# Kernel tuning notes

Hardware: AMD Instinct MI355X
Metric: run time of the kernel (lower is better)

Reference implementation:

```python
import jax, jax.numpy as jnp
import numpy as np

T, H, E, I = 2048, 2048, 8, 1408

def setup_inputs() -> dict:
    key = jax.random.key(0)
    k1, k2, k3, k4 = jax.random.split(key, 4)
    x = jax.random.normal(k1, (T, H), dtype=jnp.float32)
    gate_w = jax.random.normal(k2, (H, E), dtype=jnp.float32) * (1.0 / np.sqrt(H))
    w1 = jax.random.normal(k3, (E, H, I), dtype=jnp.float32) * (1.0 / np.sqrt(H))
    w2 = jax.random.normal(k4, (E, I, H), dtype=jnp.float32) * (1.0 / np.sqrt(I))
    return {"x": x, "gate_w": gate_w, "w1": w1, "w2": w2, "topk": 2}


def reference(x, gate_w, w1, w2, topk):
    # Router: logits -> softmax (fp32) -> top-k -> renormalize (fused_moe default)
    logits = x @ gate_w                                   # [T, E]
    probs = jax.nn.softmax(logits.astype(jnp.float32), axis=-1)
    tk_w, tk_i = jax.lax.top_k(probs, topk)               # [T, k]
    tk_w = tk_w / jnp.sum(tk_w, axis=-1, keepdims=True)
    # Scatter top-k weights into dense [T, E] combine matrix (zeros elsewhere)
    t_idx = jnp.arange(x.shape[0])[:, None]
    w_full = jnp.zeros(probs.shape, probs.dtype).at[t_idx, tk_i].set(tk_w)
    # Expert MLP: silu(x @ w1[e]) @ w2[e], combined with routing weights
    mid = jnp.einsum('th,ehi->tei', x, w1)                # [T, E, I]
    y = jnp.einsum('tei,eih->teh', jax.nn.silu(mid), w2)  # [T, E, H]
    out = jnp.einsum('te,teh->th', w_full.astype(x.dtype), y)
    return out
```

## Files before the change

### kernel.cpp

```cpp
#include <hip/hip_runtime.h>
#include <hip/hip_bf16.h>
#include <math.h>

#define TT 2048
#define HH 2048
#define EE 8
#define II 1408
#define PMAX 4608
#define MAXTILES 48

typedef short bf16x8 __attribute__((ext_vector_type(8)));
typedef float f32x4 __attribute__((ext_vector_type(4)));
typedef unsigned int u32;
typedef unsigned short u16;

__device__ __forceinline__ u16 f2bf(float f) {
  union { float f; u32 u; } v; v.f = f;
  u32 r = v.u + 0x7fffu + ((v.u >> 16) & 1u);
  return (u16)(r >> 16);
}

__device__ __forceinline__ float bf2f(u16 b) {
  union { u32 u; float f; } v; v.u = ((u32)b) << 16; return v.f;
}

__device__ __forceinline__ void gload16(const void* g, void* l) {
  __builtin_amdgcn_global_load_lds((const __attribute__((address_space(1))) u32*)g,
                                   (__attribute__((address_space(3))) u32*)l, 16, 0, 0);
}

__global__ void router_kernel(const float* __restrict__ x, const float* __restrict__ gw,
                              int* __restrict__ tk_id, float* __restrict__ tk_w) {
  int t = blockIdx.x;
  int lane = threadIdx.x;
  float acc[EE];
#pragma unroll
  for (int e = 0; e < EE; ++e) acc[e] = 0.f;
  const float* xr = x + (size_t)t * HH;
  for (int h = lane; h < HH; h += 64) {
    float xv = xr[h];
    const float* g = gw + (size_t)h * EE;
#pragma unroll
    for (int e = 0; e < EE; ++e) acc[e] += xv * g[e];
  }
#pragma unroll
  for (int off = 32; off > 0; off >>= 1) {
#pragma unroll
    for (int e = 0; e < EE; ++e) acc[e] += __shfl_down(acc[e], off, 64);
  }
  if (lane == 0) {
    int i0 = 0;
#pragma unroll
    for (int e = 1; e < EE; ++e) if (acc[e] > acc[i0]) i0 = e;
    int i1 = (i0 == 0) ? 1 : 0;
#pragma unroll
    for (int e = 0; e < EE; ++e) { if (e == i0) continue; if (acc[e] > acc[i1]) i1 = e; }
    float d = acc[i1] - acc[i0];
    float p1 = expf(d);
    float w0 = 1.f / (1.f + p1);
    float w1v = p1 * w0;
    tk_id[2 * t] = i0; tk_id[2 * t + 1] = i1;
    tk_w[2 * t] = w0;  tk_w[2 * t + 1] = w1v;
  }
}

__global__ void scanassign_kernel(const int* __restrict__ tk_id, const float* __restrict__ tk_w,
                                  int* __restrict__ offsets, int* __restrict__ poff,
                                  int* __restrict__ tok_list, float* __restrict__ wt_list,
                                  int* __restrict__ islot,
                                  int* __restrict__ t_row0, int* __restrict__ t_e,
                                  int* __restrict__ t_rlim) {
  __shared__ int s_cnt[EE];
  __shared__ int s_off[EE + 1];
  __shared__ int s_poff[EE + 1];
  __shared__ int s_cur[EE];
  int tid = threadIdx.x;
  if (tid < EE) { s_cnt[tid] = 0; s_cur[tid] = 0; }
  __syncthreads();
  for (int i = tid; i < 2 * TT; i += 256) atomicAdd(&s_cnt[tk_id[i]], 1);
  __syncthreads();
  if (tid == 0) {
    int s = 0, ps = 0;
    for (int e = 0; e < EE; ++e) {
      s_off[e] = s; s_poff[e] = ps;
      s += s_cnt[e];
      ps += ((s_cnt[e] + 63) >> 6) << 6;
    }
    s_off[EE] = s; s_poff[EE] = ps;
    for (int e = 0; e <= EE; ++e) { offsets[e] = s_off[e]; poff[e] = s_poff[e]; }
    int nt = 0;
    for (int e = 0; e < EE; ++e) {
      for (int r0 = s_poff[e]; r0 < s_poff[e + 1]; r0 += 128) {
        t_row0[nt] = r0; t_e[nt] = e; t_rlim[nt] = s_poff[e + 1]; ++nt;
      }
    }
    for (int i = nt; i < MAXTILES; ++i) t_row0[i] = -1;
  }
  __syncthreads();
  for (int t = tid; t < TT; t += 256) {
#pragma unroll
    for (int k = 0; k < 2; ++k) {
      int e = tk_id[2 * t + k];
      int p = atomicAdd(&s_cur[e], 1);
      tok_list[s_off[e] + p] = t;
      wt_list[s_off[e] + p] = tk_w[2 * t + k];
      islot[2 * t + k] = s_poff[e] + p;
    }
  }
}

__global__ void gather_x_kernel(const float* __restrict__ x, const int* __restrict__ tok_list,
                                const int* __restrict__ offsets, const int* __restrict__ poff,
                                u16* __restrict__ xg) {
  int p = blockIdx.x;
  if (p >= poff[EE]) return;
  int e = 0;
#pragma unroll
  for (int q = 1; q < EE; ++q) if (p >= poff[q]) e = q;
  int cnt = offsets[e + 1] - offsets[e];
  int r = p - poff[e]; if (r >= cnt) r = cnt - 1;
  int tok = tok_list[offsets[e] + r];
  int c = threadIdx.x * 8;
  float4 v0 = *(const float4*)(x + (size_t)tok * HH + c);
  float4 v1 = *(const float4*)(x + (size_t)tok * HH + c + 4);
  u16 o[8] = { f2bf(v0.x), f2bf(v0.y), f2bf(v0.z), f2bf(v0.w),
               f2bf(v1.x), f2bf(v1.y), f2bf(v1.z), f2bf(v1.w) };
  *(uint4*)(xg + (size_t)p * HH + c) = *(uint4*)o;
}

__global__ void convtrans_kernel(const float* __restrict__ w, u16* __restrict__ wb,
                                 int K, int N) {
  int e = blockIdx.z;
  int n0 = blockIdx.x * 64, k0 = blockIdx.y * 64;
  __shared__ u16 sT[64][72];
  const float* we = w + (size_t)e * K * N;
  u16* wbe = wb + (size_t)e * K * N;
  int tid = threadIdx.x;
  int kl = tid >> 4, n4 = tid & 15;
#pragma unroll
  for (int j = 0; j < 4; ++j) {
    int k = kl + j * 16;
    float4 v = *(const float4*)(we + (size_t)(k0 + k) * N + n0 + n4 * 4);
    sT[n4 * 4 + 0][k] = f2bf(v.x);
    sT[n4 * 4 + 1][k] = f2bf(v.y);
    sT[n4 * 4 + 2][k] = f2bf(v.z);
    sT[n4 * 4 + 3][k] = f2bf(v.w);
  }
  __syncthreads();
  int nl = tid >> 3, kc = tid & 7;
#pragma unroll
  for (int j = 0; j < 2; ++j) {
    int n = nl + j * 32;
    uint4 v = *(const uint4*)(&sT[n][kc * 8]);
    *(uint4*)(wbe + (size_t)(n0 + n) * K + k0 + kc * 8) = v;
  }
}

__global__ void combine_kernel(const u16* __restrict__ y, const int* __restrict__ islot,
                               const float* __restrict__ tk_w, float* __restrict__ out) {
  int t = blockIdx.x;
  int h = threadIdx.x * 8;
  int s0 = islot[2 * t], s1 = islot[2 * t + 1];
  float w0 = tk_w[2 * t], w1 = tk_w[2 * t + 1];
  uint4 a = *(const uint4*)(y + (size_t)s0 * HH + h);
  uint4 b = *(const uint4*)(y + (size_t)s1 * HH + h);
  const u16* ap = (const u16*)&a;
  const u16* bp = (const u16*)&b;
  float* op = out + (size_t)t * HH + h;
  float4 r0, r1;
  r0.x = w0 * bf2f(ap[0]) + w1 * bf2f(bp[0]);
  r0.y = w0 * bf2f(ap[1]) + w1 * bf2f(bp[1]);
  r0.z = w0 * bf2f(ap[2]) + w1 * bf2f(bp[2]);
  r0.w = w0 * bf2f(ap[3]) + w1 * bf2f(bp[3]);
  r1.x = w0 * bf2f(ap[4]) + w1 * bf2f(bp[4]);
  r1.y = w0 * bf2f(ap[5]) + w1 * bf2f(bp[5]);
  r1.z = w0 * bf2f(ap[6]) + w1 * bf2f(bp[6]);
  r1.w = w0 * bf2f(ap[7]) + w1 * bf2f(bp[7]);
  *(float4*)(op) = r0;
  *(float4*)(op + 4) = r1;
}

template <int KDIM, int MODE>
__launch_bounds__(256)
__global__ void moe_gemm128(const u16* __restrict__ A, const u16* __restrict__ B,
                            const int* __restrict__ t_row0, const int* __restrict__ t_e,
                            const int* __restrict__ t_rlim,
                            u16* __restrict__ midB, u16* __restrict__ y) {
  constexpr int Ndim = (MODE == 2) ? HH : II;
  constexpr int NCB = Ndim / 64;
  constexpr int NT = KDIM / 64;

  int L = blockIdx.x;
  int xcd = L & 7;
  int q = L >> 3;
  int g = q / NCB;
  int n0b = q - g * NCB;
  int ti = g * 8 + xcd;
  int row0 = t_row0[ti];
  if (row0 < 0) return;
  int e = t_e[ti];
  int rlim = t_rlim[ti];
  int n0 = n0b * 64;

  __shared__ u16 sA[128][64];
  __shared__ u16 sB[64][64];

  int tid = threadIdx.x;
  int lane = tid & 63, wv = tid >> 6;
  int wm = wv >> 1, wn = wv & 1;
  int fr = lane & 15, kg = lane >> 4;

  int rA = lane >> 3;
  int colsw = ((lane & 7) ^ rA) * 8;
  const u16* Abase = A + (size_t)(row0 + rA) * KDIM + colsw;
  const u16* Bbase = B + (size_t)e * (size_t)Ndim * KDIM + (size_t)(n0 + rA) * KDIM + colsw;

  f32x4 acc[4][2];
#pragma unroll
  for (int m = 0; m < 4; ++m)
#pragma unroll
    for (int n = 0; n < 2; ++n)
      acc[m][n] = (f32x4){0.f, 0.f, 0.f, 0.f};

  for (int t = 0; t < NT; ++t) {
    int kof = t * 64;
#pragma unroll
    for (int j = 0; j < 4; ++j) {
      int c = wv * 4 + j;
      gload16(Abase + (size_t)c * 8 * KDIM + kof, &sA[c * 8][0]);
    }
#pragma unroll
    for (int j = 0; j < 2; ++j) {
      int c = wv * 2 + j;
      gload16(Bbase + (size_t)c * 8 * KDIM + kof, &sB[c * 8][0]);
    }
    __syncthreads();
#pragma unroll
    for (int kh = 0; kh < 2; ++kh) {
      bf16x8 af[4], bg[2];
      int cbyte = (kh * 64 + kg * 16) ^ ((fr & 7) << 4);
#pragma unroll
      for (int m = 0; m < 4; ++m)
        af[m] = *(const bf16x8*)((const char*)&sA[0][0] + (wm * 64 + m * 16 + fr) * 128 + cbyte);
#pragma unroll
      for (int n = 0; n < 2; ++n)
        bg[n] = *(const bf16x8*)((const char*)&sB[0][0] + (wn * 32 + n * 16 + fr) * 128 + cbyte);
#pragma unroll
      for (int m = 0; m < 4; ++m)
#pragma unroll
        for (int n = 0; n < 2; ++n)
          acc[m][n] = __builtin_amdgcn_mfma_f32_16x16x32_bf16(af[m], bg[n], acc[m][n], 0, 0, 0);
    }
    __syncthreads();
  }

#pragma unroll
  for (int m = 0; m < 4; ++m) {
    int lr = wm * 64 + m * 16 + kg * 4;
#pragma unroll
    for (int n = 0; n < 2; ++n) {
      int lc = wn * 32 + n * 16 + fr;
#pragma unroll
      for (int r = 0; r < 4; ++r) {
        int rr = row0 + lr + r;
        if (rr < rlim) {
          if constexpr (MODE == 0) {
            float v = acc[m][n][r];
            float s = v / (1.f + expf(-v));
            midB[(size_t)rr * II + n0 + lc] = f2bf(s);
          } else {
            y[(size_t)rr * HH + n0 + lc] = f2bf(acc[m][n][r]);
          }
        }
      }
    }
  }
}

__global__ void zero_kernel(float4* __restrict__ out4, int n4) {
  int i = blockIdx.x * blockDim.x + threadIdx.x;
  int stride = gridDim.x * blockDim.x;
  float4 z; z.x = 0.f; z.y = 0.f; z.z = 0.f; z.w = 0.f;
  for (int j = i; j < n4; j += stride) out4[j] = z;
}

__launch_bounds__(256, 2)
__global__ void gemm1_small(const float* __restrict__ x, const float* __restrict__ w1,
                            const int* __restrict__ tok_list, const int* __restrict__ offsets,
                            u16* __restrict__ mid) {
  int e = blockIdx.z;
  int g_off = offsets[e];
  int n_e = offsets[e + 1] - g_off;
  int row0 = blockIdx.y * 64;
  if (row0 >= n_e) return;
  int n0 = blockIdx.x * 64;
  __shared__ u16 sA[64][72];
  __shared__ u16 sB[64][72];
  __shared__ int s_tok[64];
  int tid = threadIdx.x;
  if (tid < 64) {
    int r = row0 + tid;
    s_tok[tid] = tok_list[g_off + ((r < n_e) ? r : (n_e - 1))];
  }
  __syncthreads();
  int lane = tid & 63;
  int wv = tid >> 6;
  int wm = wv >> 1, wn = wv & 1;
  int fr = lane & 15, kg = lane >> 4;
  f32x4 acc[2][2];
#pragma unroll
  for (int i = 0; i < 2; ++i)
#pragma unroll
    for (int j = 0; j < 2; ++j) acc[i][j] = (f32x4){0.f, 0.f, 0.f, 0.f};
  const float* w1e = w1 + (size_t)e * HH * II;
  for (int k0 = 0; k0 < HH; k0 += 64) {
#pragma unroll
    for (int i = 0; i < 4; ++i) {
      int idx = tid + i * 256;
      int r = idx >> 4, c4 = idx & 15;
      float4 v = *(const float4*)(x + (size_t)s_tok[r] * HH + k0 + c4 * 4);
      unsigned long long pk = (unsigned long long)f2bf(v.x)
                            | ((unsigned long long)f2bf(v.y) << 16)
                            | ((unsigned long long)f2bf(v.z) << 32)
                            | ((unsigned long long)f2bf(v.w) << 48);
      *(unsigned long long*)(&sA[r][c4 * 4]) = pk;
    }
#pragma unroll
    for (int i = 0; i < 4; ++i) {
      int idx = tid + i * 256;
      int kk = idx >> 4, c4 = idx & 15;
      float4 v = *(const float4*)(w1e + (size_t)(k0 + kk) * II + n0 + c4 * 4);
      sB[c4 * 4 + 0][kk] = f2bf(v.x);
      sB[c4 * 4 + 1][kk] = f2bf(v.y);
      sB[c4 * 4 + 2][kk] = f2bf(v.z);
      sB[c4 * 4 + 3][kk] = f2bf(v.w);
    }
    __syncthreads();
#pragma unroll
    for (int kk = 0; kk < 64; kk += 32) {
      bf16x8 af[2], bg[2];
#pragma unroll
      for (int m = 0; m < 2; ++m) af[m] = *(const bf16x8*)(&sA[wm * 32 + m * 16 + fr][kk + kg * 8]);
#pragma unroll
      for (int n = 0; n < 2; ++n) bg[n] = *(const bf16x8*)(&sB[wn * 32 + n * 16 + fr][kk + kg * 8]);
#pragma unroll
      for (int m = 0; m < 2; ++m)
#pragma unroll
        for (int n = 0; n < 2; ++n)
          acc[m][n] = __builtin_amdgcn_mfma_f32_16x16x32_bf16(af[m], bg[n], acc[m][n], 0, 0, 0);
    }
    __syncthreads();
  }
#pragma unroll
  for (int m = 0; m < 2; ++m)
#pragma unroll
    for (int n = 0; n < 2; ++n)
#pragma unroll
      for (int r = 0; r < 4; ++r) {
        int lr = wm * 32 + m * 16 + kg * 4 + r;
        int lc = wn * 32 + n * 16 + fr;
        if (row0 + lr < n_e) {
          float v = acc[m][n][r];
          float s = v / (1.f + expf(-v));
          mid[(size_t)(g_off + row0 + lr) * II + n0 + lc] = f2bf(s);
        }
      }
}

__launch_bounds__(256, 2)
__global__ void gemm2_small(const u16* __restrict__ mid, const float* __restrict__ w2,
                            const int* __restrict__ tok_list, const float* __restrict__ wt_list,
                            const int* __restrict__ offsets, float* __restrict__ out) {
  int e = blockIdx.z;
  int g_off = offsets[e];
  int n_e = offsets[e + 1] - g_off;
  int row0 = blockIdx.y * 64;
  if (row0 >= n_e) return;
  int n0 = blockIdx.x * 64;
  __shared__ u16 sA[64][72];
  __shared__ u16 sB[64][72];
  __shared__ int s_tok[64];
  __shared__ float s_wt[64];
  int tid = threadIdx.x;
  if (tid < 64) {
    int r = row0 + tid;
    int cr = (r < n_e) ? r : (n_e - 1);
    s_tok[tid] = tok_list[g_off + cr];
    s_wt[tid] = wt_list[g_off + cr];
  }
  __syncthreads();
  int lane = tid & 63;
  int wv = tid >> 6;
  int wm = wv >> 1, wn = wv & 1;
  int fr = lane & 15, kg = lane >> 4;
  f32x4 acc[2][2];
#pragma unroll
  for (int i = 0; i < 2; ++i)
#pragma unroll
    for (int j = 0; j < 2; ++j) acc[i][j] = (f32x4){0.f, 0.f, 0.f, 0.f};
  const float* w2e = w2 + (size_t)e * II * HH;
  for (int k0 = 0; k0 < II; k0 += 64) {
#pragma unroll
    for (int i = 0; i < 2; ++i) {
      int idx = tid + i * 256;
      int r = idx >> 3, c8 = idx & 7;
      int gr = row0 + r; if (gr >= n_e) gr = n_e - 1;
      uint4 v = *(const uint4*)(mid + (size_t)(g_off + gr) * II + k0 + c8 * 8);
      *(uint4*)(&sA[r][c8 * 8]) = v;
    }
#pragma unroll
    for (int i = 0; i < 4; ++i) {
      int idx = tid + i * 256;
      int kk = idx >> 4, c4 = idx & 15;
      float4 v = *(const float4*)(w2e + (size_t)(k0 + kk) * HH + n0 + c4 * 4);
      sB[c4 * 4 + 0][kk] = f2bf(v.x);
      sB[c4 * 4 + 1][kk] = f2bf(v.y);
      sB[c4 * 4 + 2][kk] = f2bf(v.z);
      sB[c4 * 4 + 3][kk] = f2bf(v.w);
    }
    __syncthreads();
#pragma unroll
    for (int kk = 0; kk < 64; kk += 32) {
      bf16x8 af[2], bg[2];
#pragma unroll
      for (int m = 0; m < 2; ++m) af[m] = *(const bf16x8*)(&sA[wm * 32 + m * 16 + fr][kk + kg * 8]);
#pragma unroll
      for (int n = 0; n < 2; ++n) bg[n] = *(const bf16x8*)(&sB[wn * 32 + n * 16 + fr][kk + kg * 8]);
#pragma unroll
      for (int m = 0; m < 2; ++m)
#pragma unroll
        for (int n = 0; n < 2; ++n)
          acc[m][n] = __builtin_amdgcn_mfma_f32_16x16x32_bf16(af[m], bg[n], acc[m][n], 0, 0, 0);
    }
    __syncthreads();
  }
#pragma unroll
  for (int m = 0; m < 2; ++m)
#pragma unroll
    for (int n = 0; n < 2; ++n)
#pragma unroll
      for (int r = 0; r < 4; ++r) {
        int lr = wm * 32 + m * 16 + kg * 4 + r;
        int lc = wn * 32 + n * 16 + fr;
        if (row0 + lr < n_e) {
          float v = acc[m][n][r] * s_wt[lr];
          atomicAdd(out + (size_t)s_tok[lr] * HH + n0 + lc, v);
        }
      }
}

extern "C" void kernel_launch(void* const* d_in, const int* in_sizes, int n_in,
                              void* d_out, int out_size, void* d_ws, size_t ws_size,
                              hipStream_t stream) {
  const float* x  = (const float*)d_in[0];
  const float* gw = (const float*)d_in[1];
  const float* w1 = (const float*)d_in[2];
  const float* w2 = (const float*)d_in[3];
  float* out = (float*)d_out;

  char* ws = (char*)d_ws;
  int*   tk_id    = (int*)(ws);
  float* tk_w     = (float*)(ws + 16384);
  int*   offsets  = (int*)(ws + 32832);
  int*   poff     = (int*)(ws + 32896);
  int*   tok_list = (int*)(ws + 33024);
  float* wt_list  = (float*)(ws + 49408);
  int*   islot    = (int*)(ws + 65792);
  int*   t_row0   = (int*)(ws + 98304);
  int*   t_e      = (int*)(ws + 98560);
  int*   t_rlim   = (int*)(ws + 98816);

  u16* xg    = (u16*)(ws + (1u << 20));
  u16* midBp = (u16*)(ws + (20u << 20));
  u16* w1b   = (u16*)(ws + (33u << 20));
  u16* w2b   = (u16*)(ws + 80740352u);
  u16* y     = (u16*)(ws + (33u << 20));
  const size_t NEED = 126877696u;

  router_kernel<<<TT, 64, 0, stream>>>(x, gw, tk_id, tk_w);
  scanassign_kernel<<<1, 256, 0, stream>>>(tk_id, tk_w, offsets, poff, tok_list, wt_list,
                                           islot, t_row0, t_e, t_rlim);

  if (ws_size >= NEED) {
    gather_x_kernel<<<PMAX, 256, 0, stream>>>(x, tok_list, offsets, poff, xg);
    convtrans_kernel<<<dim3(II / 64, HH / 64, EE), 256, 0, stream>>>(w1, w1b, HH, II);
    convtrans_kernel<<<dim3(HH / 64, II / 64, EE), 256, 0, stream>>>(w2, w2b, II, HH);
    moe_gemm128<HH, 0><<<MAXTILES * (II / 64), 256, 0, stream>>>(
        xg, w1b, t_row0, t_e, t_rlim, midBp, y);
    moe_gemm128<II, 2><<<MAXTILES * (HH / 64), 256, 0, stream>>>(
        midBp, w2b, t_row0, t_e, t_rlim, midBp, y);
    combine_kernel<<<TT, 256, 0, stream>>>(y, islot, tk_w, out);
  } else {
    u16* mid0 = (u16*)(ws + 131072);
    zero_kernel<<<1024, 256, 0, stream>>>((float4*)out, TT * HH / 4);
    gemm1_small<<<dim3(II / 64, TT / 64, EE), 256, 0, stream>>>(x, w1, tok_list, offsets, mid0);
    gemm2_small<<<dim3(HH / 64, TT / 64, EE), 256, 0, stream>>>(mid0, w2, tok_list, wt_list, offsets, out);
  }
}
```

Baseline: 192.4 us.

## Co-schedule weight conversion with router and first GEMM in shared launches

The w1 fp32-to-bf16 transpose is merged into the router launch, and the w2 conversion is merged into the first expert GEMM launch as extra blocks. Independent work now runs concurrently and the number of kernel launches drops. The router also moves from one wave per block to four tokens per 256-thread block. The trade-off is that the GEMM1 blocks now share a launch with memory-bound conversion blocks, which can affect scheduling and occupancy.

Result: faster. 176.2 us (-8.4%).

```diff
diff --git a/kernel.cpp b/kernel.cpp
--- a/kernel.cpp
+++ b/kernel.cpp
@@ -8,6 +8,8 @@
 #define II 1408
 #define PMAX 4608
 #define MAXTILES 48
+#define G1TILES (MAXTILES * (II / 64))
+#define NCONV 5632
 
 typedef short bf16x8 __attribute__((ext_vector_type(8)));
 typedef float f32x4 __attribute__((ext_vector_type(4)));
@@ -29,38 +31,74 @@
                                    (__attribute__((address_space(3))) u32*)l, 16, 0, 0);
 }
 
-__global__ void router_kernel(const float* __restrict__ x, const float* __restrict__ gw,
-                              int* __restrict__ tk_id, float* __restrict__ tk_w) {
-  int t = blockIdx.x;
-  int lane = threadIdx.x;
-  float acc[EE];
-#pragma unroll
-  for (int e = 0; e < EE; ++e) acc[e] = 0.f;
-  const float* xr = x + (size_t)t * HH;
-  for (int h = lane; h < HH; h += 64) {
-    float xv = xr[h];
-    const float* g = gw + (size_t)h * EE;
-#pragma unroll
-    for (int e = 0; e < EE; ++e) acc[e] += xv * g[e];
-  }
-#pragma unroll
-  for (int off = 32; off > 0; off >>= 1) {
-#pragma unroll
-    for (int e = 0; e < EE; ++e) acc[e] += __shfl_down(acc[e], off, 64);
-  }
-  if (lane == 0) {
-    int i0 = 0;
-#pragma unroll
-    for (int e = 1; e < EE; ++e) if (acc[e] > acc[i0]) i0 = e;
-    int i1 = (i0 == 0) ? 1 : 0;
-#pragma unroll
-    for (int e = 0; e < EE; ++e) { if (e == i0) continue; if (acc[e] > acc[i1]) i1 = e; }
-    float d = acc[i1] - acc[i0];
-    float p1 = expf(d);
-    float w0 = 1.f / (1.f + p1);
-    float w1v = p1 * w0;
-    tk_id[2 * t] = i0; tk_id[2 * t + 1] = i1;
-    tk_w[2 * t] = w0;  tk_w[2 * t + 1] = w1v;
+__device__ __forceinline__ void conv_block(const float* __restrict__ w, u16* __restrict__ wb,
+                                           int K, int N, int b, u16* smem) {
+  int nx = N / 64, ky = K / 64;
+  int n0 = (b % nx) * 64;
+  int k0 = ((b / nx) % ky) * 64;
+  int e  = b / (nx * ky);
+  u16 (*sT)[72] = (u16(*)[72])smem;
+  const float* we = w + (size_t)e * K * N;
+  u16* wbe = wb + (size_t)e * K * N;
+  int tid = threadIdx.x;
+  int kl = tid >> 4, n4 = tid & 15;
+#pragma unroll
+  for (int j = 0; j < 4; ++j) {
+    int k = kl + j * 16;
+    float4 v = *(const float4*)(we + (size_t)(k0 + k) * N + n0 + n4 * 4);
+    sT[n4 * 4 + 0][k] = f2bf(v.x);
+    sT[n4 * 4 + 1][k] = f2bf(v.y);
+    sT[n4 * 4 + 2][k] = f2bf(v.z);
+    sT[n4 * 4 + 3][k] = f2bf(v.w);
+  }
+  __syncthreads();
+  int nl = tid >> 3, kc = tid & 7;
+#pragma unroll
+  for (int j = 0; j < 2; ++j) {
+    int n = nl + j * 32;
+    uint4 v = *(const uint4*)(&sT[n][kc * 8]);
+    *(uint4*)(wbe + (size_t)(n0 + n) * K + k0 + kc * 8) = v;
+  }
+}
+
+__global__ void router_conv_kernel(const float* __restrict__ x, const float* __restrict__ gw,
+                                   int* __restrict__ tk_id, float* __restrict__ tk_w,
+                                   const float* __restrict__ w1, u16* __restrict__ w1b) {
+  __shared__ u16 smem[64 * 72];
+  if (blockIdx.x < TT / 4) {
+    int wv = threadIdx.x >> 6, lane = threadIdx.x & 63;
+    int t = blockIdx.x * 4 + wv;
+    float acc[EE];
+#pragma unroll
+    for (int e = 0; e < EE; ++e) acc[e] = 0.f;
+    const float* xr = x + (size_t)t * HH;
+    for (int h = lane; h < HH; h += 64) {
+      float xv = xr[h];
+      const float* g = gw + (size_t)h * EE;
+#pragma unroll
+      for (int e = 0; e < EE; ++e) acc[e] += xv * g[e];
+    }
+#pragma unroll
+    for (int off = 32; off > 0; off >>= 1) {
+#pragma unroll
+      for (int e = 0; e < EE; ++e) acc[e] += __shfl_down(acc[e], off, 64);
+    }
+    if (lane == 0) {
+      int i0 = 0;
+#pragma unroll
+      for (int e = 1; e < EE; ++e) if (acc[e] > acc[i0]) i0 = e;
+      int i1 = (i0 == 0) ? 1 : 0;
+#pragma unroll
+      for (int e = 0; e < EE; ++e) { if (e == i0) continue; if (acc[e] > acc[i1]) i1 = e; }
+      float d = acc[i1] - acc[i0];
+      float p1 = expf(d);
+      float w0 = 1.f / (1.f + p1);
+      float w1v = p1 * w0;
+      tk_id[2 * t] = i0; tk_id[2 * t + 1] = i1;
+      tk_w[2 * t] = w0;  tk_w[2 * t + 1] = w1v;
+    }
+  } else {
+    conv_block(w1, w1b, HH, II, blockIdx.x - TT / 4, smem);
   }
 }
 
@@ -126,34 +164,6 @@
   u16 o[8] = { f2bf(v0.x), f2bf(v0.y), f2bf(v0.z), f2bf(v0.w),
                f2bf(v1.x), f2bf(v1.y), f2bf(v1.z), f2bf(v1.w) };
   *(uint4*)(xg + (size_t)p * HH + c) = *(uint4*)o;
-}
-
-__global__ void convtrans_kernel(const float* __restrict__ w, u16* __restrict__ wb,
-                                 int K, int N) {
-  int e = blockIdx.z;
-  int n0 = blockIdx.x * 64, k0 = blockIdx.y * 64;
-  __shared__ u16 sT[64][72];
-  const float* we = w + (size_t)e * K * N;
-  u16* wbe = wb + (size_t)e * K * N;
-  int tid = threadIdx.x;
-  int kl = tid >> 4, n4 = tid & 15;
-#pragma unroll
-  for (int j = 0; j < 4; ++j) {
-    int k = kl + j * 16;
-    float4 v = *(const float4*)(we + (size_t)(k0 + k) * N + n0 + n4 * 4);
-    sT[n4 * 4 + 0][k] = f2bf(v.x);
-    sT[n4 * 4 + 1][k] = f2bf(v.y);
-    sT[n4 * 4 + 2][k] = f2bf(v.z);
-    sT[n4 * 4 + 3][k] = f2bf(v.w);
-  }
-  __syncthreads();
-  int nl = tid >> 3, kc = tid & 7;
-#pragma unroll
-  for (int j = 0; j < 2; ++j) {
-    int n = nl + j * 32;
-    uint4 v = *(const uint4*)(&sT[n][kc * 8]);
-    *(uint4*)(wbe + (size_t)(n0 + n) * K + k0 + kc * 8) = v;
-  }
 }
 
 __global__ void combine_kernel(const u16* __restrict__ y, const int* __restrict__ islot,
@@ -180,14 +190,109 @@
   *(float4*)(op + 4) = r1;
 }
 
-template <int KDIM, int MODE>
+__global__ void gemm1_conv_kernel(const u16* __restrict__ A, const u16* __restrict__ B,
+                                  const int* __restrict__ t_row0, const int* __restrict__ t_e,
+                                  const int* __restrict__ t_rlim,
+                                  u16* __restrict__ midB,
+                                  const float* __restrict__ w2, u16* __restrict__ w2b) {
+  __shared__ u16 smem[12288];
+  if (blockIdx.x >= G1TILES) {
+    conv_block(w2, w2b, II, HH, blockIdx.x - G1TILES, smem);
+    return;
+  }
+  constexpr int KDIM = HH;
+  constexpr int NCB = II / 64;
+  constexpr int NT = KDIM / 64;
+
+  int L = blockIdx.x;
+  int xcd = L & 7;
+  int q = L >> 3;
+  int g = q / NCB;
+  int n0b = q - g * NCB;
+  int ti = g * 8 + xcd;
+  int row0 = t_row0[ti];
+  if (row0 < 0) return;
+  int rlim = t_rlim[ti];
+  int e = t_e[ti];
+  int n0 = n0b * 64;
+
+  u16 (*sA)[64] = (u16(*)[64])smem;
+  u16 (*sB)[64] = (u16(*)[64])(smem + 8192);
+
+  int tid = threadIdx.x;
+  int lane = tid & 63, wv = tid >> 6;
+  int wm = wv >> 1, wn = wv & 1;
+  int fr = lane & 15, kg = lane >> 4;
+
+  int rA = lane >> 3;
+  int colsw = ((lane & 7) ^ rA) * 8;
+  const u16* Abase = A + (size_t)(row0 + rA) * KDIM + colsw;
+  const u16* Bbase = B + (size_t)e * (size_t)II * KDIM + (size_t)(n0 + rA) * KDIM + colsw;
+
+  f32x4 acc[4][2];
+#pragma unroll
+  for (int m = 0; m < 4; ++m)
+#pragma unroll
+    for (int n = 0; n < 2; ++n)
+      acc[m][n] = (f32x4){0.f, 0.f, 0.f, 0.f};
+
+  for (int t = 0; t < NT; ++t) {
+    int kof = t * 64;
+#pragma unroll
+    for (int j = 0; j < 4; ++j) {
+      int c = wv * 4 + j;
+      gload16(Abase + (size_t)c * 8 * KDIM + kof, &sA[c * 8][0]);
+    }
+#pragma unroll
+    for (int j = 0; j < 2; ++j) {
+      int c = wv * 2 + j;
+      gload16(Bbase + (size_t)c * 8 * KDIM + kof, &sB[c * 8][0]);
+    }
+    __syncthreads();
+#pragma unroll
+    for (int kh = 0; kh < 2; ++kh) {
+      bf16x8 af[4], bg[2];
+      int cbyte = (kh * 64 + kg * 16) ^ ((fr & 7) << 4);
+#pragma unroll
+      for (int m = 0; m < 4; ++m)
+        af[m] = *(const bf16x8*)((const char*)&sA[0][0] + (wm * 64 + m * 16 + fr) * 128 + cbyte);
+#pragma unroll
+      for (int n = 0; n < 2; ++n)
+        bg[n] = *(const bf16x8*)((const char*)&sB[0][0] + (wn * 32 + n * 16 + fr) * 128 + cbyte);
+#pragma unroll
+      for (int m = 0; m < 4; ++m)
+#pragma unroll
+        for (int n = 0; n < 2; ++n)
+          acc[m][n] = __builtin_amdgcn_mfma_f32_16x16x32_bf16(af[m], bg[n], acc[m][n], 0, 0, 0);
+    }
+    __syncthreads();
+  }
+
+#pragma unroll
+  for (int m = 0; m < 4; ++m) {
+    int lr = wm * 64 + m * 16 + kg * 4;
+#pragma unroll
+    for (int n = 0; n < 2; ++n) {
+      int lc = wn * 32 + n * 16 + fr;
+#pragma unroll
+      for (int r = 0; r < 4; ++r) {
+        int rr = row0 + lr + r;
+        if (rr < rlim) {
+          float v = acc[m][n][r];
+          float s = v / (1.f + expf(-v));
+          midB[(size_t)rr * II + n0 + lc] = f2bf(s);
+        }
+      }
+    }
+  }
+}
+
 __launch_bounds__(256)
-__global__ void moe_gemm128(const u16* __restrict__ A, const u16* __restrict__ B,
-                            const int* __restrict__ t_row0, const int* __restrict__ t_e,
-                            const int* __restrict__ t_rlim,
-                            u16* __restrict__ midB, u16* __restrict__ y) {
-  constexpr int Ndim = (MODE == 2) ? HH : II;
-  constexpr int NCB = Ndim / 64;
+__global__ void moe_gemm2(const u16* __restrict__ A, const u16* __restrict__ B,
+                          const int* __restrict__ t_row0, const int* __restrict__ t_e,
+                          const int* __restrict__ t_rlim, u16* __restrict__ y) {
+  constexpr int KDIM = II;
+  constexpr int NCB = HH / 64;
   constexpr int NT = KDIM / 64;
 
   int L = blockIdx.x;
@@ -213,7 +318,7 @@
   int rA = lane >> 3;
   int colsw = ((lane & 7) ^ rA) * 8;
   const u16* Abase = A + (size_t)(row0 + rA) * KDIM + colsw;
-  const u16* Bbase = B + (size_t)e * (size_t)Ndim * KDIM + (size_t)(n0 + rA) * KDIM + colsw;
+  const u16* Bbase = B + (size_t)e * (size_t)HH * KDIM + (size_t)(n0 + rA) * KDIM + colsw;
 
   f32x4 acc[4][2];
 #pragma unroll
@@ -263,15 +368,8 @@
 #pragma unroll
       for (int r = 0; r < 4; ++r) {
         int rr = row0 + lr + r;
-        if (rr < rlim) {
-          if constexpr (MODE == 0) {
-            float v = acc[m][n][r];
-            float s = v / (1.f + expf(-v));
-            midB[(size_t)rr * II + n0 + lc] = f2bf(s);
-          } else {
-            y[(size_t)rr * HH + n0 + lc] = f2bf(acc[m][n][r]);
-          }
-        }
+        if (rr < rlim)
+          y[(size_t)rr * HH + n0 + lc] = f2bf(acc[m][n][r]);
       }
     }
   }
@@ -282,6 +380,41 @@
   int stride = gridDim.x * blockDim.x;
   float4 z; z.x = 0.f; z.y = 0.f; z.z = 0.f; z.w = 0.f;
   for (int j = i; j < n4; j += stride) out4[j] = z;
+}
+
+__global__ void router_kernel(const float* __restrict__ x, const float* __restrict__ gw,
+                              int* __restrict__ tk_id, float* __restrict__ tk_w) {
+  int t = blockIdx.x;
+  int lane = threadIdx.x;
+  float acc[EE];
+#pragma unroll
+  for (int e = 0; e < EE; ++e) acc[e] = 0.f;
+  const float* xr = x + (size_t)t * HH;
+  for (int h = lane; h < HH; h += 64) {
+    float xv = xr[h];
+    const float* g = gw + (size_t)h * EE;
+#pragma unroll
+    for (int e = 0; e < EE; ++e) acc[e] += xv * g[e];
+  }
+#pragma unroll
+  for (int off = 32; off > 0; off >>= 1) {
+#pragma unroll
+    for (int e = 0; e < EE; ++e) acc[e] += __shfl_down(acc[e], off, 64);
+  }
+  if (lane == 0) {
+    int i0 = 0;
+#pragma unroll
+    for (int e = 1; e < EE; ++e) if (acc[e] > acc[i0]) i0 = e;
+    int i1 = (i0 == 0) ? 1 : 0;
+#pragma unroll
+    for (int e = 0; e < EE; ++e) { if (e == i0) continue; if (acc[e] > acc[i1]) i1 = e; }
+    float d = acc[i1] - acc[i0];
+    float p1 = expf(d);
+    float w0 = 1.f / (1.f + p1);
+    float w1v = p1 * w0;
+    tk_id[2 * t] = i0; tk_id[2 * t + 1] = i1;
+    tk_w[2 * t] = w0;  tk_w[2 * t + 1] = w1v;
+  }
 }
 
 __launch_bounds__(256, 2)
@@ -477,21 +610,22 @@
   u16* y     = (u16*)(ws + (33u << 20));
   const size_t NEED = 126877696u;
 
-  router_kernel<<<TT, 64, 0, stream>>>(x, gw, tk_id, tk_w);
-  scanassign_kernel<<<1, 256, 0, stream>>>(tk_id, tk_w, offsets, poff, tok_list, wt_list,
-                                           islot, t_row0, t_e, t_rlim);
-
   if (ws_size >= NEED) {
+    router_conv_kernel<<<TT / 4 + NCONV, 256, 0, stream>>>(x, gw, tk_id, tk_w, w1, w1b);
+    scanassign_kernel<<<1, 256, 0, stream>>>(tk_id, tk_w, offsets, poff, tok_list, wt_list,
+                                             islot, t_row0, t_e, t_rlim);
     gather_x_kernel<<<PMAX, 256, 0, stream>>>(x, tok_list, offsets, poff, xg);
-    convtrans_kernel<<<dim3(II / 64, HH / 64, EE), 256, 0, stream>>>(w1, w1b, HH, II);
-    convtrans_kernel<<<dim3(HH / 64, II / 64, EE), 256, 0, stream>>>(w2, w2b, II, HH);
-    moe_gemm128<HH, 0><<<MAXTILES * (II / 64), 256, 0, stream>>>(
-        xg, w1b, t_row0, t_e, t_rlim, midBp, y);
-    moe_gemm128<II, 2><<<MAXTILES * (HH / 64), 256, 0, stream>>>(
-        midBp, w2b, t_row0, t_e, t_rlim, midBp, y);
+    gemm1_conv_kernel<<<G1TILES + NCONV, 256, 0, stream>>>(
+        xg, w1b, t_row0, t_e, t_rlim, midBp, w2, w2b);
+    moe_gemm2<<<MAXTILES * (HH / 64), 256, 0, stream>>>(
+        midBp, w2b, t_row0, t_e, t_rlim, y);
     combine_kernel<<<TT, 256, 0, stream>>>(y, islot, tk_w, out);
   } else {
+    int*   tk_id2 = tk_id; float* tk_w2 = tk_w;
     u16* mid0 = (u16*)(ws + 131072);
+    router_kernel<<<TT, 64, 0, stream>>>(x, gw, tk_id2, tk_w2);
+    scanassign_kernel<<<1, 256, 0, stream>>>(tk_id2, tk_w2, offsets, poff, tok_list, wt_list,
+                                             islot, t_row0, t_e, t_rlim);
     zero_kernel<<<1024, 256, 0, stream>>>((float4*)out, TT * HH / 4);
     gemm1_small<<<dim3(II / 64, TT / 64, EE), 256, 0, stream>>>(x, w1, tok_list, offsets, mid0);
     gemm2_small<<<dim3(HH / 64, TT / 64, EE), 256, 0, stream>>>(mid0, w2, tok_list, wt_list, offsets, out);
```

## Overlap weight conversion with router and split expert GEMMs into staggered kernels

Applied to the files above, without the earlier changes.

Merges the router with the w1 bf16 convert/transpose into one launch, and the w2 conversion with GEMM1 for experts 0-3. GEMM1 for experts 4-7 then runs alongside GEMM2 for experts 0-3, and a final kernel does GEMM2 for experts 4-7. The goal is to fill idle CUs and cut kernel boundaries by running independent work in the same grid. Heterogeneous blocks share one shared-memory size and register budget, which can lower occupancy. The expert split also depends on how tokens are spread across experts.

After: 188.0 us. 1.02x faster.

```diff
diff --git a/kernel.cpp b/kernel.cpp
--- a/kernel.cpp
+++ b/kernel.cpp
@@ -8,6 +8,10 @@
 #define II 1408
 #define PMAX 4608
 #define MAXTILES 48
+#define G1TILES (MAXTILES * (II / 64))
+#define G2TILES (MAXTILES * (HH / 64))
+#define NCONV 5632
+#define ESPLIT 4
 
 typedef short bf16x8 __attribute__((ext_vector_type(8)));
 typedef float f32x4 __attribute__((ext_vector_type(4)));
@@ -29,38 +33,172 @@
                                    (__attribute__((address_space(3))) u32*)l, 16, 0, 0);
 }
 
-__global__ void router_kernel(const float* __restrict__ x, const float* __restrict__ gw,
-                              int* __restrict__ tk_id, float* __restrict__ tk_w) {
-  int t = blockIdx.x;
-  int lane = threadIdx.x;
-  float acc[EE];
-#pragma unroll
-  for (int e = 0; e < EE; ++e) acc[e] = 0.f;
-  const float* xr = x + (size_t)t * HH;
-  for (int h = lane; h < HH; h += 64) {
-    float xv = xr[h];
-    const float* g = gw + (size_t)h * EE;
-#pragma unroll
-    for (int e = 0; e < EE; ++e) acc[e] += xv * g[e];
-  }
-#pragma unroll
-  for (int off = 32; off > 0; off >>= 1) {
-#pragma unroll
-    for (int e = 0; e < EE; ++e) acc[e] += __shfl_down(acc[e], off, 64);
-  }
-  if (lane == 0) {
-    int i0 = 0;
-#pragma unroll
-    for (int e = 1; e < EE; ++e) if (acc[e] > acc[i0]) i0 = e;
-    int i1 = (i0 == 0) ? 1 : 0;
-#pragma unroll
-    for (int e = 0; e < EE; ++e) { if (e == i0) continue; if (acc[e] > acc[i1]) i1 = e; }
-    float d = acc[i1] - acc[i0];
-    float p1 = expf(d);
-    float w0 = 1.f / (1.f + p1);
-    float w1v = p1 * w0;
-    tk_id[2 * t] = i0; tk_id[2 * t + 1] = i1;
-    tk_w[2 * t] = w0;  tk_w[2 * t + 1] = w1v;
+__device__ __forceinline__ void conv_block(const float* __restrict__ w, u16* __restrict__ wb,
+                                           int K, int N, int b, u16* smem) {
+  int nx = N / 64, ky = K / 64;
+  int n0 = (b % nx) * 64;
+  int k0 = ((b / nx) % ky) * 64;
+  int e  = b / (nx * ky);
+  u16 (*sT)[76] = (u16(*)[76])smem;
+  const float* we = w + (size_t)e * K * N;
+  u16* wbe = wb + (size_t)e * K * N;
+  int tid = threadIdx.x;
+  int kl = tid >> 4, n4 = tid & 15;
+#pragma unroll
+  for (int j = 0; j < 4; ++j) {
+    int k = kl + j * 16;
+    float4 v = *(const float4*)(we + (size_t)(k0 + k) * N + n0 + n4 * 4);
+    sT[n4 * 4 + 0][k] = f2bf(v.x);
+    sT[n4 * 4 + 1][k] = f2bf(v.y);
+    sT[n4 * 4 + 2][k] = f2bf(v.z);
+    sT[n4 * 4 + 3][k] = f2bf(v.w);
+  }
+  __syncthreads();
+  int nl = tid >> 3, kc = tid & 7;
+#pragma unroll
+  for (int j = 0; j < 2; ++j) {
+    int n = nl + j * 32;
+    uint4 v = *(const uint4*)(&sT[n][kc * 8]);
+    *(uint4*)(wbe + (size_t)(n0 + n) * K + k0 + kc * 8) = v;
+  }
+}
+
+template <int KDIM, int MODE, int ELO, int EHI>
+__device__ __forceinline__ void gemm128_body(int L, const u16* __restrict__ A,
+                                             const u16* __restrict__ B,
+                                             const int* __restrict__ t_row0,
+                                             const int* __restrict__ t_e,
+                                             const int* __restrict__ t_rlim,
+                                             u16* __restrict__ outp, u16* smem) {
+  constexpr int Ndim = (MODE == 2) ? HH : II;
+  constexpr int NCB = Ndim / 64;
+  constexpr int NT = KDIM / 64;
+
+  int xcd = L & 7;
+  int q = L >> 3;
+  int g = q / NCB;
+  int n0b = q - g * NCB;
+  int ti = g * 8 + xcd;
+  int row0 = t_row0[ti];
+  if (row0 < 0) return;
+  int e = t_e[ti];
+  if (e < ELO || e >= EHI) return;
+  int rlim = t_rlim[ti];
+  int n0 = n0b * 64;
+
+  u16 (*sA)[64] = (u16(*)[64])smem;
+  u16 (*sB)[64] = (u16(*)[64])(smem + 8192);
+
+  int tid = threadIdx.x;
+  int lane = tid & 63, wv = tid >> 6;
+  int wm = wv >> 1, wn = wv & 1;
+  int fr = lane & 15, kg = lane >> 4;
+
+  int rA = lane >> 3;
+  int colsw = ((lane & 7) ^ rA) * 8;
+  const u16* Abase = A + (size_t)(row0 + rA) * KDIM + colsw;
+  const u16* Bbase = B + (size_t)e * (size_t)Ndim * KDIM + (size_t)(n0 + rA) * KDIM + colsw;
+
+  f32x4 acc[4][2];
+#pragma unroll
+  for (int m = 0; m < 4; ++m)
+#pragma unroll
+    for (int n = 0; n < 2; ++n)
+      acc[m][n] = (f32x4){0.f, 0.f, 0.f, 0.f};
+
+  for (int t = 0; t < NT; ++t) {
+    int kof = t * 64;
+#pragma unroll
+    for (int j = 0; j < 4; ++j) {
+      int c = wv * 4 + j;
+      gload16(Abase + (size_t)c * 8 * KDIM + kof, &sA[c * 8][0]);
+    }
+#pragma unroll
+    for (int j = 0; j < 2; ++j) {
+      int c = wv * 2 + j;
+      gload16(Bbase + (size_t)c * 8 * KDIM + kof, &sB[c * 8][0]);
+    }
+    __syncthreads();
+#pragma unroll
+    for (int kh = 0; kh < 2; ++kh) {
+      bf16x8 af[4], bg[2];
+      int cbyte = (kh * 64 + kg * 16) ^ ((fr & 7) << 4);
+#pragma unroll
+      for (int m = 0; m < 4; ++m)
+        af[m] = *(const bf16x8*)((const char*)&sA[0][0] + (wm * 64 + m * 16 + fr) * 128 + cbyte);
+#pragma unroll
+      for (int n = 0; n < 2; ++n)
+        bg[n] = *(const bf16x8*)((const char*)&sB[0][0] + (wn * 32 + n * 16 + fr) * 128 + cbyte);
+#pragma unroll
+      for (int m = 0; m < 4; ++m)
+#pragma unroll
+        for (int n = 0; n < 2; ++n)
+          acc[m][n] = __builtin_amdgcn_mfma_f32_16x16x32_bf16(af[m], bg[n], acc[m][n], 0, 0, 0);
+    }
+    __syncthreads();
+  }
+
+#pragma unroll
+  for (int m = 0; m < 4; ++m) {
+    int lr = wm * 64 + m * 16 + kg * 4;
+#pragma unroll
+    for (int n = 0; n < 2; ++n) {
+      int lc = wn * 32 + n * 16 + fr;
+#pragma unroll
+      for (int r = 0; r < 4; ++r) {
+        int rr = row0 + lr + r;
+        if (rr < rlim) {
+          if constexpr (MODE == 0) {
+            float v = acc[m][n][r];
+            float s = v / (1.f + expf(-v));
+            outp[(size_t)rr * II + n0 + lc] = f2bf(s);
+          } else {
+            outp[(size_t)rr * HH + n0 + lc] = f2bf(acc[m][n][r]);
+          }
+        }
+      }
+    }
+  }
+}
+
+__global__ void router_conv_kernel(const float* __restrict__ x, const float* __restrict__ gw,
+                                   int* __restrict__ tk_id, float* __restrict__ tk_w,
+                                   const float* __restrict__ w1, u16* __restrict__ w1b) {
+  __shared__ u16 smem[64 * 76];
+  if (blockIdx.x < TT / 4) {
+    int wv = threadIdx.x >> 6, lane = threadIdx.x & 63;
+    int t = blockIdx.x * 4 + wv;
+    float acc[EE];
+#pragma unroll
+    for (int e = 0; e < EE; ++e) acc[e] = 0.f;
+    const float* xr = x + (size_t)t * HH;
+    for (int h = lane; h < HH; h += 64) {
+      float xv = xr[h];
+      const float* g = gw + (size_t)h * EE;
+#pragma unroll
+      for (int e = 0; e < EE; ++e) acc[e] += xv * g[e];
+    }
+#pragma unroll
+    for (int off = 32; off > 0; off >>= 1) {
+#pragma unroll
+      for (int e = 0; e < EE; ++e) acc[e] += __shfl_down(acc[e], off, 64);
+    }
+    if (lane == 0) {
+      int i0 = 0;
+#pragma unroll
+      for (int e = 1; e < EE; ++e) if (acc[e] > acc[i0]) i0 = e;
+      int i1 = (i0 == 0) ? 1 : 0;
+#pragma unroll
+      for (int e = 0; e < EE; ++e) { if (e == i0) continue; if (acc[e] > acc[i1]) i1 = e; }
+      float d = acc[i1] - acc[i0];
+      float p1 = expf(d);
+      float w0 = 1.f / (1.f + p1);
+      float w1v = p1 * w0;
+      tk_id[2 * t] = i0; tk_id[2 * t + 1] = i1;
+      tk_w[2 * t] = w0;  tk_w[2 * t + 1] = w1v;
+    }
+  } else {
+    conv_block(w1, w1b, HH, II, blockIdx.x - TT / 4, smem);
   }
 }
 
@@ -128,32 +266,37 @@
   *(uint4*)(xg + (size_t)p * HH + c) = *(uint4*)o;
 }
 
-__global__ void convtrans_kernel(const float* __restrict__ w, u16* __restrict__ wb,
-                                 int K, int N) {
-  int e = blockIdx.z;
-  int n0 = blockIdx.x * 64, k0 = blockIdx.y * 64;
-  __shared__ u16 sT[64][72];
-  const float* we = w + (size_t)e * K * N;
-  u16* wbe = wb + (size_t)e * K * N;
-  int tid = threadIdx.x;
-  int kl = tid >> 4, n4 = tid & 15;
-#pragma unroll
-  for (int j = 0; j < 4; ++j) {
-    int k = kl + j * 16;
-    float4 v = *(const float4*)(we + (size_t)(k0 + k) * N + n0 + n4 * 4);
-    sT[n4 * 4 + 0][k] = f2bf(v.x);
-    sT[n4 * 4 + 1][k] = f2bf(v.y);
-    sT[n4 * 4 + 2][k] = f2bf(v.z);
-    sT[n4 * 4 + 3][k] = f2bf(v.w);
-  }
-  __syncthreads();
-  int nl = tid >> 3, kc = tid & 7;
-#pragma unroll
-  for (int j = 0; j < 2; ++j) {
-    int n = nl + j * 32;
-    uint4 v = *(const uint4*)(&sT[n][kc * 8]);
-    *(uint4*)(wbe + (size_t)(n0 + n) * K + k0 + kc * 8) = v;
-  }
+__global__ void k4a_kernel(const u16* __restrict__ xg, const u16* __restrict__ w1b,
+                           const int* __restrict__ t_row0, const int* __restrict__ t_e,
+                           const int* __restrict__ t_rlim, u16* __restrict__ midB,
+                           const float* __restrict__ w2, u16* __restrict__ w2b) {
+  __shared__ u16 smem[12288];
+  if (blockIdx.x >= G1TILES) {
+    conv_block(w2, w2b, II, HH, blockIdx.x - G1TILES, smem);
+    return;
+  }
+  gemm128_body<HH, 0, 0, ESPLIT>(blockIdx.x, xg, w1b, t_row0, t_e, t_rlim, midB, smem);
+}
+
+__global__ void k4b_kernel(const u16* __restrict__ xg, const u16* __restrict__ w1b,
+                           u16* __restrict__ midB, const u16* __restrict__ w2b,
+                           u16* __restrict__ y,
+                           const int* __restrict__ t_row0, const int* __restrict__ t_e,
+                           const int* __restrict__ t_rlim) {
+  __shared__ u16 smem[12288];
+  if (blockIdx.x < G1TILES) {
+    gemm128_body<HH, 0, ESPLIT, EE>(blockIdx.x, xg, w1b, t_row0, t_e, t_rlim, midB, smem);
+  } else {
+    gemm128_body<II, 2, 0, ESPLIT>(blockIdx.x - G1TILES, midB, w2b, t_row0, t_e, t_rlim, y, smem);
+  }
+}
+
+__global__ void k5_kernel(const u16* __restrict__ midB, const u16* __restrict__ w2b,
+                          u16* __restrict__ y,
+                          const int* __restrict__ t_row0, const int* __restrict__ t_e,
+                          const int* __restrict__ t_rlim) {
+  __shared__ u16 smem[12288];
+  gemm128_body<II, 2, ESPLIT, EE>(blockIdx.x, midB, w2b, t_row0, t_e, t_rlim, y, smem);
 }
 
 __global__ void combine_kernel(const u16* __restrict__ y, const int* __restrict__ islot,
@@ -180,108 +323,46 @@
   *(float4*)(op + 4) = r1;
 }
 
-template <int KDIM, int MODE>
-__launch_bounds__(256)
-__global__ void moe_gemm128(const u16* __restrict__ A, const u16* __restrict__ B,
-                            const int* __restrict__ t_row0, const int* __restrict__ t_e,
-                            const int* __restrict__ t_rlim,
-                            u16* __restrict__ midB, u16* __restrict__ y) {
-  constexpr int Ndim = (MODE == 2) ? HH : II;
-  constexpr int NCB = Ndim / 64;
-  constexpr int NT = KDIM / 64;
-
-  int L = blockIdx.x;
-  int xcd = L & 7;
-  int q = L >> 3;
-  int g = q / NCB;
-  int n0b = q - g * NCB;
-  int ti = g * 8 + xcd;
-  int row0 = t_row0[ti];
-  if (row0 < 0) return;
-  int e = t_e[ti];
-  int rlim = t_rlim[ti];
-  int n0 = n0b * 64;
-
-  __shared__ u16 sA[128][64];
-  __shared__ u16 sB[64][64];
-
-  int tid = threadIdx.x;
-  int lane = tid & 63, wv = tid >> 6;
-  int wm = wv >> 1, wn = wv & 1;
-  int fr = lane & 15, kg = lane >> 4;
-
-  int rA = lane >> 3;
-  int colsw = ((lane & 7) ^ rA) * 8;
-  const u16* Abase = A + (size_t)(row0 + rA) * KDIM + colsw;
-  const u16* Bbase = B + (size_t)e * (size_t)Ndim * KDIM + (size_t)(n0 + rA) * KDIM + colsw;
-
-  f32x4 acc[4][2];
-#pragma unroll
-  for (int m = 0; m < 4; ++m)
-#pragma unroll
-    for (int n = 0; n < 2; ++n)
-      acc[m][n] = (f32x4){0.f, 0.f, 0.f, 0.f};
-
-  for (int t = 0; t < NT; ++t) {
-    int kof = t * 64;
-#pragma unroll
-    for (int j = 0; j < 4; ++j) {
-      int c = wv * 4 + j;
-      gload16(Abase + (size_t)c * 8 * KDIM + kof, &sA[c * 8][0]);
-    }
-#pragma unroll
-    for (int j = 0; j < 2; ++j) {
-      int c = wv * 2 + j;
-      gload16(Bbase + (size_t)c * 8 * KDIM + kof, &sB[c * 8][0]);
-    }
-    __syncthreads();
-#pragma unroll
-    for (int kh = 0; kh < 2; ++kh) {
-      bf16x8 af[4], bg[2];
-      int cbyte = (kh * 64 + kg * 16) ^ ((fr & 7) << 4);
-#pragma unroll
-      for (int m = 0; m < 4; ++m)
-        af[m] = *(const bf16x8*)((const char*)&sA[0][0] + (wm * 64 + m * 16 + fr) * 128 + cbyte);
-#pragma unroll
-      for (int n = 0; n < 2; ++n)
-        bg[n] = *(const bf16x8*)((const char*)&sB[0][0] + (wn * 32 + n * 16 + fr) * 128 + cbyte);
-#pragma unroll
-      for (int m = 0; m < 4; ++m)
-#pragma unroll
-        for (int n = 0; n < 2; ++n)
-          acc[m][n] = __builtin_amdgcn_mfma_f32_16x16x32_bf16(af[m], bg[n], acc[m][n], 0, 0, 0);
-    }
-    __syncthreads();
-  }
-
-#pragma unroll
-  for (int m = 0; m < 4; ++m) {
-    int lr = wm * 64 + m * 16 + kg * 4;
-#pragma unroll
-    for (int n = 0; n < 2; ++n) {
-      int lc = wn * 32 + n * 16 + fr;
-#pragma unroll
-      for (int r = 0; r < 4; ++r) {
-        int rr = row0 + lr + r;
-        if (rr < rlim) {
-          if constexpr (MODE == 0) {
-            float v = acc[m][n][r];
-            float s = v / (1.f + expf(-v));
-            midB[(size_t)rr * II + n0 + lc] = f2bf(s);
-          } else {
-            y[(size_t)rr * HH + n0 + lc] = f2bf(acc[m][n][r]);
-          }
-        }
-      }
-    }
-  }
-}
-
 __global__ void zero_kernel(float4* __restrict__ out4, int n4) {
   int i = blockIdx.x * blockDim.x + threadIdx.x;
   int stride = gridDim.x * blockDim.x;
   float4 z; z.x = 0.f; z.y = 0.f; z.z = 0.f; z.w = 0.f;
   for (int j = i; j < n4; j += stride) out4[j] = z;
+}
+
+__global__ void router_kernel(const float* __restrict__ x, const float* __restrict__ gw,
+                              int* __restrict__ tk_id, float* __restrict__ tk_w) {
+  int t = blockIdx.x;
+  int lane = threadIdx.x;
+  float acc[EE];
+#pragma unroll
+  for (int e = 0; e < EE; ++e) acc[e] = 0.f;
+  const float* xr = x + (size_t)t * HH;
+  for (int h = lane; h < HH; h += 64) {
+    float xv = xr[h];
+    const float* g = gw + (size_t)h * EE;
+#pragma unroll
+    for (int e = 0; e < EE; ++e) acc[e] += xv * g[e];
+  }
+#pragma unroll
+  for (int off = 32; off > 0; off >>= 1) {
+#pragma unroll
+    for (int e = 0; e < EE; ++e) acc[e] += __shfl_down(acc[e], off, 64);
+  }
+  if (lane == 0) {
+    int i0 = 0;
+#pragma unroll
+    for (int e = 1; e < EE; ++e) if (acc[e] > acc[i0]) i0 = e;
+    int i1 = (i0 == 0) ? 1 : 0;
+#pragma unroll
+    for (int e = 0; e < EE; ++e) { if (e == i0) continue; if (acc[e] > acc[i1]) i1 = e; }
+    float d = acc[i1] - acc[i0];
+    float p1 = expf(d);
+    float w0 = 1.f / (1.f + p1);
+    float w1v = p1 * w0;
+    tk_id[2 * t] = i0; tk_id[2 * t + 1] = i1;
+    tk_w[2 * t] = w0;  tk_w[2 * t + 1] = w1v;
+  }
 }
 
 __launch_bounds__(256, 2)
@@ -477,21 +558,22 @@
   u16* y     = (u16*)(ws + (33u << 20));
   const size_t NEED = 126877696u;
 
-  router_kernel<<<TT, 64, 0, stream>>>(x, gw, tk_id, tk_w);
-  scanassign_kernel<<<1, 256, 0, stream>>>(tk_id, tk_w, offsets, poff, tok_list, wt_list,
-                                           islot, t_row0, t_e, t_rlim);
-
   if (ws_size >= NEED) {
+    router_conv_kernel<<<TT / 4 + NCONV, 256, 0, stream>>>(x, gw, tk_id, tk_w, w1, w1b);
+    scanassign_kernel<<<1, 256, 0, stream>>>(tk_id, tk_w, offsets, poff, tok_list, wt_list,
+                                             islot, t_row0, t_e, t_rlim);
     gather_x_kernel<<<PMAX, 256, 0, stream>>>(x, tok_list, offsets, poff, xg);
-    convtrans_kernel<<<dim3(II / 64, HH / 64, EE), 256, 0, stream>>>(w1, w1b, HH, II);
-    convtrans_kernel<<<dim3(HH / 64, II / 64, EE), 256, 0, stream>>>(w2, w2b, II, HH);
-    moe_gemm128<HH, 0><<<MAXTILES * (II / 64), 256, 0, stream>>>(
-        xg, w1b, t_row0, t_e, t_rlim, midBp, y);
-    moe_gemm128<II, 2><<<MAXTILES * (HH / 64), 256, 0, stream>>>(
-        midBp, w2b, t_row0, t_e, t_rlim, midBp, y);
+    k4a_kernel<<<G1TILES + NCONV, 256, 0, stream>>>(
+        xg, w1b, t_row0, t_e, t_rlim, midBp, w2, w2b);
+    k4b_kernel<<<G1TILES + G2TILES, 256, 0, stream>>>(
+        xg, w1b, midBp, w2b, y, t_row0, t_e, t_rlim);
+    k5_kernel<<<G2TILES, 256, 0, stream>>>(midBp, w2b, y, t_row0, t_e, t_rlim);
     combine_kernel<<<TT, 256, 0, stream>>>(y, islot, tk_w, out);
   } else {
     u16* mid0 = (u16*)(ws + 131072);
+    router_kernel<<<TT, 64, 0, stream>>>(x, gw, tk_id, tk_w);
+    scanassign_kernel<<<1, 256, 0, stream>>>(tk_id, tk_w, offsets, poff, tok_list, wt_list,
+                                             islot, t_row0, t_e, t_rlim);
     zero_kernel<<<1024, 256, 0, stream>>>((float4*)out, TT * HH / 4);
     gemm1_small<<<dim3(II / 64, TT / 64, EE), 256, 0, stream>>>(x, w1, tok_list, offsets, mid0);
     gemm2_small<<<dim3(HH / 64, TT / 64, EE), 256, 0, stream>>>(mid0, w2, tok_list, wt_list, offsets, out);
```
